# Kernel tuning notes

Hardware: AMD Instinct MI355X
Metric: run time of the kernel (lower is better)

Reference implementation:

```python
import jax, jax.numpy as jnp
import numpy as np

N, E, DIM = 50000, 500000, 64
EIN3, EIN4 = 16, 16

def setup_inputs() -> dict:
    key = jax.random.key(0)
    ks = jax.random.split(key, 8)
    x = jax.random.normal(ks[0], (N, DIM), dtype=jnp.float32)
    edge_index3 = jax.random.randint(ks[1], (2, E), 0, N, dtype=jnp.int64)
    edge_attr3 = jax.random.normal(ks[2], (E, EIN3), dtype=jnp.float32)
    edge_attr4 = jax.random.normal(ks[3], (E, EIN4), dtype=jnp.float32)
    batch = jnp.zeros((N,), dtype=jnp.int64)
    # MLP params: Linear(2*dim, 4*dim) -> ReLU -> Linear(4*dim, 1)
    W1 = jax.random.normal(ks[4], (2 * DIM, 4 * DIM), dtype=jnp.float32) / np.sqrt(2 * DIM)
    b1 = jnp.zeros((4 * DIM,), dtype=jnp.float32)
    W2 = jax.random.normal(ks[5], (4 * DIM, 1), dtype=jnp.float32) / np.sqrt(4 * DIM)
    b2 = jnp.zeros((1,), dtype=jnp.float32)
    return {"x": x, "edge_index3": edge_index3, "edge_attr3": edge_attr3,
            "edge_attr4": edge_attr4, "batch": batch,
            "W1": W1, "b1": b1, "W2": W2, "b2": b2}

def reference(x, edge_index3, edge_attr3, edge_attr4, batch, W1, b1, W2, b2):
    # gather endpoints: temp[k] = x[edge_index3[k]] -> [E, dim]
    src = x[edge_index3[0]]  # [E, dim]
    dst = x[edge_index3[1]]  # [E, dim]
    # symmetric concat: [[src|dst], [dst|src]] -> [2E, 2*dim]
    yhat = jnp.concatenate([
        jnp.concatenate([src, dst], axis=1),
        jnp.concatenate([dst, src], axis=1)], axis=0)
    h = jax.nn.relu(yhat @ W1 + b1)        # [2E, 4*dim]
    y = (h @ W2 + b2)[:, 0]                # [2E]
    return y.reshape(2, -1).mean(axis=0)   # [E]
```

## Files before the change

### kernel.cpp

```cpp
#include <hip/hip_runtime.h>

#define DIM 64
#define HID 256
#define ROWB 512
#define QSCALE  25.4f
#define DQSCALE (5.0f/127.0f)

typedef short s8v  __attribute__((ext_vector_type(8)));
typedef float f4v  __attribute__((ext_vector_type(4)));
typedef float f2v  __attribute__((ext_vector_type(2)));
typedef unsigned short u16x2 __attribute__((ext_vector_type(2)));

union U16 { uint4 u; s8v s; };

__device__ __forceinline__ unsigned short bf16_rne(float f) {
    unsigned u = __float_as_uint(f);
    u = (u + 0x7fffu + ((u >> 16) & 1u)) >> 16;
    return (unsigned short)u;
}
__device__ __forceinline__ unsigned pk_bf16(float a, float b) {
    return (unsigned)bf16_rne(a) | ((unsigned)bf16_rne(b) << 16);
}

__device__ __forceinline__ u16x2 as_u16x2(unsigned v) { union { unsigned u; u16x2 s; } c; c.u = v; return c.s; }
__device__ __forceinline__ unsigned as_u32(u16x2 v)   { union { u16x2 s; unsigned u; } c; c.s = v; return c.u; }

#define DPP_ADD(x, ctrl, rmask)                                               \
    (x) += __int_as_float(__builtin_amdgcn_update_dpp(                        \
        0, __float_as_int(x), (ctrl), (rmask), 0xf, true))

__global__ __launch_bounds__(256) void prep_wfrag(
    const float* __restrict__ W1, unsigned short* __restrict__ wf)
{
    const int f = blockIdx.x * 256 + threadIdx.x;
    if (f >= 32 * 2 * 64) return;
    const int lane = f & 63;
    const int t    = (f >> 6) & 1;
    const int ct   = f >> 7;
    const int col  = ct * 16 + (lane & 15);
    const int k0   = t * 32 + (lane >> 4) * 8;
    const float* __restrict__ wsrc =
        W1 + ((col >= HID) ? (DIM * HID + col - HID) : col);
    unsigned short v[8];
#pragma unroll
    for (int j = 0; j < 8; ++j) v[j] = bf16_rne(wsrc[(size_t)(k0 + j) * HID]);
    uint4 o;
    o.x = (unsigned)v[0] | ((unsigned)v[1] << 16);
    o.y = (unsigned)v[2] | ((unsigned)v[3] << 16);
    o.z = (unsigned)v[4] | ((unsigned)v[5] << 16);
    o.w = (unsigned)v[6] | ((unsigned)v[7] << 16);
    *(uint4*)(wf + (size_t)f * 8) = o;
}

__global__ __launch_bounds__(256) void node_mfma_q(
    const float* __restrict__ x, const unsigned short* __restrict__ wf,
    const float* __restrict__ b1, unsigned char* __restrict__ tab, int n)
{
    const int lane    = threadIdx.x & 63;
    const int w       = threadIdx.x >> 6;
    const int rowgrp  = w >> 1;
    const int colhalf = w & 1;
    const int m       = lane & 15;
    const int quad    = lane >> 4;
    const int rbase   = blockIdx.x * 32 + rowgrp * 16;

    const int arow = rbase + m;
    const float* __restrict__ xr = x + (size_t)((arow < n) ? arow : (n - 1)) * DIM;
    s8v a[2];
#pragma unroll
    for (int t = 0; t < 2; ++t) {
        const float4 lo = *(const float4*)(xr + t * 32 + quad * 8);
        const float4 hi = *(const float4*)(xr + t * 32 + quad * 8 + 4);
        U16 u;
        u.u.x = pk_bf16(lo.x, lo.y);
        u.u.y = pk_bf16(lo.z, lo.w);
        u.u.z = pk_bf16(hi.x, hi.y);
        u.u.w = pk_bf16(hi.z, hi.w);
        a[t] = u.s;
    }

    const uint4* __restrict__ wfv = (const uint4*)wf;

    f4v acc[16];
#pragma unroll
    for (int ct = 0; ct < 16; ++ct) {
        const int ctg = colhalf * 16 + ct;
        U16 b0u, b1u;
        b0u.u = wfv[(ctg * 2 + 0) * 64 + lane];
        b1u.u = wfv[(ctg * 2 + 1) * 64 + lane];
        f4v c = {0.f, 0.f, 0.f, 0.f};
        c = __builtin_amdgcn_mfma_f32_16x16x32_bf16(a[0], b0u.s, c, 0, 0, 0);
        c = __builtin_amdgcn_mfma_f32_16x16x32_bf16(a[1], b1u.s, c, 0, 0, 0);
        if (colhalf == 0) {
            const float bias = b1[ctg * 16 + m];
            c[0] += bias; c[1] += bias; c[2] += bias; c[3] += bias;
        }
        acc[ct] = c;
    }

#pragma unroll
    for (int r = 0; r < 4; ++r) {
        const int gr = rbase + quad * 4 + r;
        if (gr >= n) continue;
        unsigned b[16];
#pragma unroll
        for (int ct = 0; ct < 16; ++ct) {
            float v = __builtin_rintf(acc[ct][r] * QSCALE);
            v = fminf(fmaxf(v, -127.f), 127.f);
            b[ct] = (unsigned)((int)v + 127);
        }
        uint4 o;
        o.x = b[0]  | (b[1]  << 8) | (b[2]  << 16) | (b[3]  << 24);
        o.y = b[4]  | (b[5]  << 8) | (b[6]  << 16) | (b[7]  << 24);
        o.z = b[8]  | (b[9]  << 8) | (b[10] << 16) | (b[11] << 24);
        o.w = b[12] | (b[13] << 8) | (b[14] << 16) | (b[15] << 24);
        *(uint4*)(tab + (size_t)gr * ROWB + colhalf * 256 + m * 16) = o;
    }
}

__device__ __forceinline__ float pass_dot(const uint4 S, const uint4 D,
                                          const f2v* __restrict__ w)
{
    const unsigned sa[4] = {S.x, S.y, S.z, S.w};
    const unsigned da[4] = {D.x, D.y, D.z, D.w};
    const u16x2 k254 = {254, 254};
    f2v acc; acc.x = 0.f; acc.y = 0.f;
#pragma unroll
    for (int i = 0; i < 4; ++i) {
        const unsigned zs0 = __builtin_amdgcn_perm(0u, sa[i], 0x0C010C00u);
        const unsigned zs1 = __builtin_amdgcn_perm(0u, sa[i], 0x0C030C02u);
        const unsigned zd0 = __builtin_amdgcn_perm(0u, da[i], 0x0C010C00u);
        const unsigned zd1 = __builtin_amdgcn_perm(0u, da[i], 0x0C030C02u);
        const unsigned r0 = as_u32(__builtin_elementwise_sub_sat(
                                as_u16x2(zs0) + as_u16x2(zd0), k254));
        const unsigned r1 = as_u32(__builtin_elementwise_sub_sat(
                                as_u16x2(zs1) + as_u16x2(zd1), k254));
        f2v f0, f1;
        f0.x = (float)(r0 & 0xffu);
        f0.y = (float)((r0 >> 16) & 0xffu);
        f1.x = (float)(r1 & 0xffu);
        f1.y = (float)((r1 >> 16) & 0xffu);
        acc = f0 * w[2 * i] + acc;
        acc = f1 * w[2 * i + 1] + acc;
    }
    return acc.x + acc.y;
}

__global__ __launch_bounds__(256, 8) void edge_mlp_q(
    const int* __restrict__ ei, const unsigned char* __restrict__ tab,
    const float* __restrict__ W2, const float* __restrict__ b2,
    float* __restrict__ out, int ne)
{
    const int lane = threadIdx.x & 63;
    const int l31  = lane & 31;
    const int m    = lane & 15;
    const bool hi  = lane >= 32;

    f2v w[8];
#pragma unroll
    for (int i = 0; i < 4; ++i) {
        f2v w0, w1;
        w0.x = W2[(4 * i + 0) * 16 + m]; w0.y = W2[(4 * i + 1) * 16 + m];
        w1.x = W2[(4 * i + 2) * 16 + m]; w1.y = W2[(4 * i + 3) * 16 + m];
        w[2 * i] = w0; w[2 * i + 1] = w1;
    }
    const float bias = b2[0];
    const float sc   = 0.5f * DQSCALE;

    const unsigned offS = 16u * (unsigned)l31;
    const unsigned offD = 16u * (unsigned)(l31 ^ 16);

    const int wflat = __builtin_amdgcn_readfirstlane(
        (int)(blockIdx.x * 4 + (threadIdx.x >> 6)));
    const int nw = (int)gridDim.x * 4;
    const int ng = ne >> 3;
    const int gq = ng / nw, gr = ng % nw;
    int g        = wflat * gq + (wflat < gr ? wflat : gr);
    const int ge = g + gq + (wflat < gr ? 1 : 0);

    for (; g < ge; ++g) {
        const int e0 = __builtin_amdgcn_readfirstlane(g << 3);
        int se[8], de[8];
#pragma unroll
        for (int i = 0; i < 8; ++i) {
            se[i] = ei[e0 + i];
            de[i] = ei[ne + e0 + i];
        }

        uint4 S, D, Sn, Dn;
        {
            const unsigned vs = ((unsigned)(hi ? se[1] : se[0]) << 9) + offS;
            const unsigned vd = ((unsigned)(hi ? de[1] : de[0]) << 9) + offD;
            S = *(const uint4*)(tab + vs);
            D = *(const uint4*)(tab + vd);
        }
#pragma unroll
        for (int p = 0; p < 4; ++p) {
            if (p < 3) {
                const unsigned vs = ((unsigned)(hi ? se[2*p+3] : se[2*p+2]) << 9) + offS;
                const unsigned vd = ((unsigned)(hi ? de[2*p+3] : de[2*p+2]) << 9) + offD;
                Sn = *(const uint4*)(tab + vs);
                Dn = *(const uint4*)(tab + vd);
            }
            float s = pass_dot(S, D, w);
            DPP_ADD(s, 0x111, 0xf);
            DPP_ADD(s, 0x112, 0xf);
            DPP_ADD(s, 0x114, 0xf);
            DPP_ADD(s, 0x118, 0xf);
            DPP_ADD(s, 0x142, 0xa);
            if (l31 == 31) out[e0 + 2 * p + (lane >> 5)] = fmaf(sc, s, bias);
            S = Sn; D = Dn;
        }
    }

    const int rem = ne & 7;
    if (rem && wflat == 0) {
        const int base = ne & ~7;
#pragma unroll
        for (int p = 0; p < 4; ++p) {
            const int eA = base + 2 * p;
            if (eA < ne) {
                const int eB = (eA + 1 < ne) ? eA + 1 : eA;
                const unsigned vs = ((unsigned)(hi ? ei[eB] : ei[eA]) << 9) + offS;
                const unsigned vd = ((unsigned)(hi ? ei[ne + eB] : ei[ne + eA]) << 9) + offD;
                const uint4 St = *(const uint4*)(tab + vs);
                const uint4 Dt = *(const uint4*)(tab + vd);
                float s = pass_dot(St, Dt, w);
                DPP_ADD(s, 0x111, 0xf);
                DPP_ADD(s, 0x112, 0xf);
                DPP_ADD(s, 0x114, 0xf);
                DPP_ADD(s, 0x118, 0xf);
                DPP_ADD(s, 0x142, 0xa);
                const int e = eA + (lane >> 5);
                if (l31 == 31 && e < ne) out[e] = fmaf(sc, s, bias);
            }
        }
    }
}

extern "C" void kernel_launch(void* const* d_in, const int* in_sizes, int n_in,
                              void* d_out, int out_size, void* d_ws, size_t ws_size,
                              hipStream_t stream) {
    const float* x  = (const float*)d_in[0];
    const int*   ei = (const int*)d_in[1];
    const float* W1 = (const float*)d_in[5];
    const float* b1 = (const float*)d_in[6];
    const float* W2 = (const float*)d_in[7];
    const float* b2 = (const float*)d_in[8];
    float* out = (float*)d_out;

    const int n  = in_sizes[0] / DIM;
    const int ne = in_sizes[1] / 2;

    unsigned char*  tab = (unsigned char*)d_ws;
    unsigned short* wf  = (unsigned short*)(tab + (size_t)n * ROWB);

    prep_wfrag<<<16, 256, 0, stream>>>(W1, wf);
    node_mfma_q<<<(n + 31) / 32, 256, 0, stream>>>(x, wf, b1, tab, n);
    edge_mlp_q<<<2048, 256, 0, stream>>>(ei, tab, W2, b2, out, ne);
}
```

Measured before the change: 192.0 us.

## Grid-stride edge loop with 4 edges per wave and larger grid

Replaces the contiguous per-wave chunk of 8-edge groups, which used software-pipelined prefetch of table rows, with a grid-stride loop. Each wave now handles 4 edges per iteration and issues all four gathers at once. The edge kernel grid grows from 2048 to 8192 blocks. The aim is to raise occupancy and memory-level parallelism across waves instead of relying on in-wave prefetching. The cost is less latency hiding within a wave and a serial tail loop.

```diff
diff --git a/kernel.cpp b/kernel.cpp
--- a/kernel.cpp
+++ b/kernel.cpp
@@ -28,6 +28,13 @@
 #define DPP_ADD(x, ctrl, rmask)                                               \
     (x) += __int_as_float(__builtin_amdgcn_update_dpp(                        \
         0, __float_as_int(x), (ctrl), (rmask), 0xf, true))
+#define DPP_REDUCE5(x) do {                                                   \
+    DPP_ADD(x, 0x111, 0xf);                                                   \
+    DPP_ADD(x, 0x112, 0xf);                                                   \
+    DPP_ADD(x, 0x114, 0xf);                                                   \
+    DPP_ADD(x, 0x118, 0xf);                                                   \
+    DPP_ADD(x, 0x142, 0xa);                                                   \
+} while (0)
 
 __global__ __launch_bounds__(256) void prep_wfrag(
     const float* __restrict__ W1, unsigned short* __restrict__ wf)
@@ -170,70 +177,42 @@
     const unsigned offS = 16u * (unsigned)l31;
     const unsigned offD = 16u * (unsigned)(l31 ^ 16);
 
-    const int wflat = __builtin_amdgcn_readfirstlane(
-        (int)(blockIdx.x * 4 + (threadIdx.x >> 6)));
-    const int nw = (int)gridDim.x * 4;
-    const int ng = ne >> 3;
-    const int gq = ng / nw, gr = ng % nw;
-    int g        = wflat * gq + (wflat < gr ? wflat : gr);
-    const int ge = g + gq + (wflat < gr ? 1 : 0);
-
-    for (; g < ge; ++g) {
-        const int e0 = __builtin_amdgcn_readfirstlane(g << 3);
-        int se[8], de[8];
-#pragma unroll
-        for (int i = 0; i < 8; ++i) {
-            se[i] = ei[e0 + i];
-            de[i] = ei[ne + e0 + i];
-        }
-
-        uint4 S, D, Sn, Dn;
-        {
-            const unsigned vs = ((unsigned)(hi ? se[1] : se[0]) << 9) + offS;
-            const unsigned vd = ((unsigned)(hi ? de[1] : de[0]) << 9) + offD;
-            S = *(const uint4*)(tab + vs);
-            D = *(const uint4*)(tab + vd);
-        }
-#pragma unroll
-        for (int p = 0; p < 4; ++p) {
-            if (p < 3) {
-                const unsigned vs = ((unsigned)(hi ? se[2*p+3] : se[2*p+2]) << 9) + offS;
-                const unsigned vd = ((unsigned)(hi ? de[2*p+3] : de[2*p+2]) << 9) + offD;
-                Sn = *(const uint4*)(tab + vs);
-                Dn = *(const uint4*)(tab + vd);
-            }
-            float s = pass_dot(S, D, w);
-            DPP_ADD(s, 0x111, 0xf);
-            DPP_ADD(s, 0x112, 0xf);
-            DPP_ADD(s, 0x114, 0xf);
-            DPP_ADD(s, 0x118, 0xf);
-            DPP_ADD(s, 0x142, 0xa);
-            if (l31 == 31) out[e0 + 2 * p + (lane >> 5)] = fmaf(sc, s, bias);
-            S = Sn; D = Dn;
-        }
-    }
-
-    const int rem = ne & 7;
-    if (rem && wflat == 0) {
-        const int base = ne & ~7;
-#pragma unroll
-        for (int p = 0; p < 4; ++p) {
-            const int eA = base + 2 * p;
-            if (eA < ne) {
-                const int eB = (eA + 1 < ne) ? eA + 1 : eA;
-                const unsigned vs = ((unsigned)(hi ? ei[eB] : ei[eA]) << 9) + offS;
-                const unsigned vd = ((unsigned)(hi ? ei[ne + eB] : ei[ne + eA]) << 9) + offD;
-                const uint4 St = *(const uint4*)(tab + vs);
-                const uint4 Dt = *(const uint4*)(tab + vd);
-                float s = pass_dot(St, Dt, w);
-                DPP_ADD(s, 0x111, 0xf);
-                DPP_ADD(s, 0x112, 0xf);
-                DPP_ADD(s, 0x114, 0xf);
-                DPP_ADD(s, 0x118, 0xf);
-                DPP_ADD(s, 0x142, 0xa);
-                const int e = eA + (lane >> 5);
-                if (l31 == 31 && e < ne) out[e] = fmaf(sc, s, bias);
-            }
+    const int wid = blockIdx.x * 4 + (threadIdx.x >> 6);
+    const int nw  = (int)gridDim.x * 4;
+    const int ne4 = ne & ~3;
+
+    for (int e0 = wid * 4; e0 < ne4; e0 += nw * 4) {
+        const int eu = __builtin_amdgcn_readfirstlane(e0);
+        const int s0 = ei[eu],          s1 = ei[eu + 1];
+        const int s2 = ei[eu + 2],      s3 = ei[eu + 3];
+        const int d0 = ei[ne + eu],     d1 = ei[ne + eu + 1];
+        const int d2 = ei[ne + eu + 2], d3 = ei[ne + eu + 3];
+
+        const uint4 T0 = *(const uint4*)(tab + (((unsigned)(hi ? s1 : s0)) << 9) + offS);
+        const uint4 T1 = *(const uint4*)(tab + (((unsigned)(hi ? d1 : d0)) << 9) + offD);
+        const uint4 T2 = *(const uint4*)(tab + (((unsigned)(hi ? s3 : s2)) << 9) + offS);
+        const uint4 T3 = *(const uint4*)(tab + (((unsigned)(hi ? d3 : d2)) << 9) + offD);
+
+        float r0 = pass_dot(T0, T1, w);
+        DPP_REDUCE5(r0);
+        float r1 = pass_dot(T2, T3, w);
+        DPP_REDUCE5(r1);
+
+        if (l31 == 31) {
+            const int eo = eu + (lane >> 5);
+            out[eo]     = fmaf(sc, r0, bias);
+            out[eo + 2] = fmaf(sc, r1, bias);
+        }
+    }
+
+    if ((ne & 3) && wid == 0) {
+        for (int e = ne4; e < ne; ++e) {
+            const int s = ei[e], d = ei[ne + e];
+            const uint4 S = *(const uint4*)(tab + ((unsigned)s << 9) + offS);
+            const uint4 D = *(const uint4*)(tab + ((unsigned)d << 9) + offD);
+            float r = pass_dot(S, D, w);
+            DPP_REDUCE5(r);
+            if (lane == 31) out[e] = fmaf(sc, r, bias);
         }
     }
 }
@@ -257,5 +236,5 @@
 
     prep_wfrag<<<16, 256, 0, stream>>>(W1, wf);
     node_mfma_q<<<(n + 31) / 32, 256, 0, stream>>>(x, wf, b1, tab, n);
-    edge_mlp_q<<<2048, 256, 0, stream>>>(ei, tab, W2, b2, out, ne);
-}
+    edge_mlp_q<<<8192, 256, 0, stream>>>(ei, tab, W2, b2, out, ne);
+}
```

After: 187.3 us. 1.03x faster.
